# Kernel tuning notes

Hardware: AMD Instinct MI355X
Metric: run time of the kernel (lower is better)

## Reference

```python
import jax, jax.numpy as jnp
import numpy as np

N_NODES = 20000
NEG_SLOPE = 0.2  # PyG GATConv default leaky_relu slope


def segment_softmax(e, dst, num_segments):
    # e: [E, H] edge logits, softmax over edges sharing the same dst node
    m = jax.ops.segment_max(e, dst, num_segments=num_segments)
    ex = jnp.exp(e - m[dst])
    s = jax.ops.segment_sum(ex, dst, num_segments=num_segments)
    return ex / (s[dst] + 1e-16)


def gat_conv(x, src, dst, W, att_src, att_dst, bias, concat):
    # PyG GATConv (add_self_loops handled by caller). W: [Fin, H*C], att_*: [H, C]
    N = x.shape[0]
    H, C = att_src.shape
    h = (x @ W).reshape(N, H, C)
    a_src = jnp.einsum('nhc,hc->nh', h, att_src)  # [N, H]
    a_dst = jnp.einsum('nhc,hc->nh', h, att_dst)
    e = jax.nn.leaky_relu(a_src[src] + a_dst[dst], NEG_SLOPE)  # [E, H]
    alpha = segment_softmax(e, dst, N)
    msg = alpha[:, :, None] * h[src]  # [E, H, C]
    out = jax.ops.segment_sum(msg, dst, num_segments=N)  # [N, H, C]
    out = out.reshape(N, H * C) if concat else out.mean(axis=1)
    return out + bias


def add_self_loops(edge_index, num_nodes):
    loops = jnp.arange(num_nodes, dtype=edge_index.dtype)
    src = jnp.concatenate([edge_index[0], loops])
    dst = jnp.concatenate([edge_index[1], loops])
    return src, dst


def setup_inputs() -> dict:
    key = jax.random.key(0)
    ks = jax.random.split(key, 24)
    Fin, Hd, Hh, C2, Md = 1280, 256, 4, 128, 1024

    def w(k, shape, fan_in):
        return (jax.random.normal(k, shape, jnp.float32) * (1.0 / np.sqrt(fan_in))).astype(jnp.float32)

    return {
        'x': jax.random.normal(ks[0], (N_NODES, Fin), jnp.float32),
        'edge_index': jax.random.randint(ks[1], (2, 200000), 0, N_NODES, jnp.int32),
        'mutation_idx': 12345,
        'mutation_site_diff': jax.random.normal(ks[2], (1, Md), jnp.float32),
        # mutation_diff_processor: 1024 -> 128 -> 128
        'W_mut1': w(ks[3], (Md, 128), Md), 'b_mut1': jnp.zeros((128,), jnp.float32),
        'W_mut2': w(ks[4], (128, 128), 128), 'b_mut2': jnp.zeros((128,), jnp.float32),
        # GATConv1: Fin -> 256, 4 heads, concat
        'gat1_W': w(ks[5], (Fin, Hh * Hd), Fin),
        'gat1_as': w(ks[6], (Hh, Hd), Hd), 'gat1_ad': w(ks[7], (Hh, Hd), Hd),
        'gat1_b': jnp.zeros((Hh * Hd,), jnp.float32),
        # GATConv2: 1024 -> 128, 1 head
        'gat2_W': w(ks[8], (Hh * Hd, C2), Hh * Hd),
        'gat2_as': w(ks[9], (1, C2), C2), 'gat2_ad': w(ks[10], (1, C2), C2),
        'gat2_b': jnp.zeros((C2,), jnp.float32),
        # binding_predictor: 256 -> 128 -> 32 -> 1
        'W_p1': w(ks[11], (C2 + 128, 128), C2 + 128), 'b_p1': jnp.zeros((128,), jnp.float32),
        'W_p2': w(ks[12], (128, 32), 128), 'b_p2': jnp.zeros((32,), jnp.float32),
        'W_p3': w(ks[13], (32, 1), 32), 'b_p3': jnp.zeros((1,), jnp.float32),
    }


def reference(x, edge_index, mutation_idx, mutation_site_diff,
              W_mut1, b_mut1, W_mut2, b_mut2,
              gat1_W, gat1_as, gat1_ad, gat1_b,
              gat2_W, gat2_as, gat2_ad, gat2_b,
              W_p1, b_p1, W_p2, b_p2, W_p3, b_p3):
    src, dst = add_self_loops(edge_index, x.shape[0])
    # mutation diff MLP (dropout = identity at eval)
    pmd = jax.nn.relu(mutation_site_diff @ W_mut1 + b_mut1) @ W_mut2 + b_mut2
    h = jax.nn.relu(gat_conv(x, src, dst, gat1_W, gat1_as, gat1_ad, gat1_b, concat=True))
    h = jax.nn.relu(gat_conv(h, src, dst, gat2_W, gat2_as, gat2_ad, gat2_b, concat=False))
    feat = h[mutation_idx:mutation_idx + 1]  # [1, 128]
    z = jnp.concatenate([feat, pmd], axis=-1)
    z = jax.nn.relu(z @ W_p1 + b_p1)
    z = jax.nn.relu(z @ W_p2 + b_p2)
    return z @ W_p3 + b_p3
```

## Files before the change

### kernel.cpp

```cpp
#include <hip/hip_runtime.h>
#include <hip/hip_bf16.h>

#define NNODES 20000
#define NE_RAW 200000
#define NE_TOT 220000
#define MAX1   128
#define MAX2   512
#define MAXE1  4096
#define MAXE2  256
#define FIN    1280
#define FH     1024
#define HC     256
#define NHEAD  4
#define C2     128
#define CAPE   512
#define GB_HH  544
#define GB_GB  128

__device__ __forceinline__ float lrelu(float x){ return x >= 0.f ? x : 0.2f * x; }

__device__ __forceinline__ float blockSum(float v, float* red4){
  #pragma unroll
  for (int o = 32; o; o >>= 1) v += __shfl_xor(v, o, 64);
  int t = threadIdx.x;
  __syncthreads();
  if ((t & 63) == 0) red4[t >> 6] = v;
  __syncthreads();
  return red4[0] + red4[1] + red4[2] + red4[3];
}

__global__ void k_init(int* cnt, int* slot1, int* slot2){
  int i = blockIdx.x * 256 + threadIdx.x;
  if (i < NNODES){ slot1[i] = -1; slot2[i] = -1; }
  if (i < 8) cnt[i] = 0;
}

__global__ void k_scan1(const int* __restrict__ ei, const int* __restrict__ mip,
                        int* cnt, int* slot1, int* S1, int* E2){
  int e = blockIdx.x * 256 + threadIdx.x;
  if (e >= NE_TOT) return;
  int mi = mip[0];
  int src, dst;
  if (e < NE_RAW){ src = ei[e]; dst = ei[NE_RAW + e]; }
  else { src = e - NE_RAW; dst = src; }
  if (dst != mi) return;
  int p = atomicAdd(&cnt[3], 1);
  if (p < MAXE2) E2[p] = src;
  if (atomicCAS(&slot1[src], -1, -9) == -1){
    int idx = atomicAdd(&cnt[0], 1);
    if (idx < MAX1){ S1[idx] = src; slot1[src] = idx; }
  }
}

__global__ void k_scan2(const int* __restrict__ ei, int* cnt,
                        const int* __restrict__ slot1, int* slot2,
                        int* S2, int* E1s, int* E1d){
  int e = blockIdx.x * 256 + threadIdx.x;
  if (e >= NE_TOT) return;
  int src, dst;
  if (e < NE_RAW){ src = ei[e]; dst = ei[NE_RAW + e]; }
  else { src = e - NE_RAW; dst = src; }
  if (slot1[dst] < 0) return;
  int p = atomicAdd(&cnt[2], 1);
  if (p < MAXE1){ E1s[p] = src; E1d[p] = dst; }
  if (atomicCAS(&slot2[src], -1, -9) == -1){
    int idx = atomicAdd(&cnt[1], 1);
    if (idx < MAX2){ S2[idx] = src; slot2[src] = idx; }
  }
}

__global__ __launch_bounds__(256) void k_hh(
    const float* __restrict__ x, const float* __restrict__ W1,
    const float* __restrict__ msd, const float* __restrict__ Wm1,
    const float* __restrict__ bm1,
    const int* __restrict__ cnt, const int* __restrict__ S2,
    float* __restrict__ hh, float* __restrict__ r1){
  int t = threadIdx.x;
  if (blockIdx.x >= GB_HH){
    __shared__ float red[256];
    int b   = blockIdx.x - GB_HH;
    int col = b * 32 + (t & 31);
    int sl  = t >> 5;
    float p = 0.f;
    for (int k = sl * 128; k < sl * 128 + 128; ++k)
      p += msd[k] * Wm1[k * C2 + col];
    red[t] = p;
    __syncthreads();
    if (t < 32){
      float s = 0.f;
      #pragma unroll
      for (int q = 0; q < 8; ++q) s += red[q * 32 + t];
      float v = s + bm1[col];
      r1[col] = v > 0.f ? v : 0.f;
    }
    return;
  }
  __shared__ float xs[8 * 160];
  int n2 = cnt[1]; if (n2 > MAX2) n2 = MAX2;
  int nRG = (n2 + 7) >> 3;
  int nT  = nRG * 32;
  for (int task = blockIdx.x; task < nT; task += GB_HH){
    int rg  = task >> 5;
    int rem = task & 31;
    int ct  = rem >> 3;
    int kc  = rem & 7;
    int r0  = rg * 8;
    int nr  = n2 - r0; if (nr > 8) nr = 8;
    int k0  = kc * 160;
    __syncthreads();
    for (int idx = t; idx < 8 * 40; idx += 256){
      int r = idx / 40, k4 = idx - r * 40;
      float4 v = make_float4(0.f, 0.f, 0.f, 0.f);
      if (r < nr)
        v = *(const float4*)(x + (long)S2[r0 + r] * FIN + k0 + k4 * 4);
      *(float4*)(xs + r * 160 + k4 * 4) = v;
    }
    __syncthreads();
    int col = ct * 256 + t;
    float acc[8] = {0.f,0.f,0.f,0.f,0.f,0.f,0.f,0.f};
    const float* Wp = W1 + (long)k0 * FH + col;
    #pragma unroll 4
    for (int kk = 0; kk < 160; ++kk){
      float w = Wp[(long)kk * FH];
      #pragma unroll
      for (int r = 0; r < 8; ++r) acc[r] += xs[r * 160 + kk] * w;
    }
    #pragma unroll
    for (int r = 0; r < 8; ++r)
      if (r < nr) atomicAdd(hh + (long)(r0 + r) * FH + col, acc[r]);
  }
}

__global__ void k_ascal(const float* __restrict__ hh,
                        const float* __restrict__ as1, const float* __restrict__ ad1,
                        const int* __restrict__ cnt,
                        float* __restrict__ asrc1, float* __restrict__ adst1){
  int t = threadIdx.x, w = t >> 6, lane = t & 63;
  int n2 = cnt[1]; if (n2 > MAX2) n2 = MAX2;
  for (int i = blockIdx.x; i < n2; i += gridDim.x){
    const float* row = hh + (long)i * FH + w * HC;
    float ss = 0.f, sd = 0.f;
    #pragma unroll
    for (int q = 0; q < 4; ++q){
      float v = row[q * 64 + lane];
      ss += v * as1[w * HC + q * 64 + lane];
      sd += v * ad1[w * HC + q * 64 + lane];
    }
    #pragma unroll
    for (int o = 32; o; o >>= 1){
      ss += __shfl_xor(ss, o, 64);
      sd += __shfl_xor(sd, o, 64);
    }
    if (lane == 0){ asrc1[i * NHEAD + w] = ss; adst1[i * NHEAD + w] = sd; }
  }
}

__global__ void k_agg1(const float* __restrict__ hh,
                       const float* __restrict__ asrc1, const float* __restrict__ adst1,
                       const float* __restrict__ b1,
                       const int* __restrict__ cnt, const int* __restrict__ S1,
                       const int* __restrict__ slot2,
                       const int* __restrict__ E1s, const int* __restrict__ E1d,
                       float* __restrict__ h1){
  __shared__ int   lsrc[CAPE];
  __shared__ float ev[CAPE];
  __shared__ int   scnt;
  int t = threadIdx.x;
  int n1  = cnt[0]; if (n1  > MAX1)  n1  = MAX1;
  int nE1 = cnt[2]; if (nE1 > MAXE1) nE1 = MAXE1;
  int nT = n1 * NHEAD;
  for (int task = blockIdx.x; task < nT; task += gridDim.x){
    int j = task >> 2, hd = task & 3;
    int s = S1[j];
    __syncthreads();
    if (t == 0) scnt = 0;
    __syncthreads();
    for (int e = t; e < nE1; e += 256){
      if (E1d[e] == s){
        int p = atomicAdd(&scnt, 1);
        if (p < CAPE) lsrc[p] = slot2[E1s[e]];
      }
    }
    __syncthreads();
    int ce = scnt; if (ce > CAPE) ce = CAPE;
    if (t < 64){
      float ad = adst1[slot2[s] * NHEAD + hd];
      float m = -3.4e38f;
      for (int e = t; e < ce; e += 64){
        float v = lrelu(asrc1[lsrc[e] * NHEAD + hd] + ad);
        ev[e] = v;
        m = fmaxf(m, v);
      }
      #pragma unroll
      for (int o = 32; o; o >>= 1) m = fmaxf(m, __shfl_xor(m, o, 64));
      float ssum = 0.f;
      for (int e = t; e < ce; e += 64){
        float a = expf(ev[e] - m);
        ev[e] = a;
        ssum += a;
      }
      #pragma unroll
      for (int o = 32; o; o >>= 1) ssum += __shfl_xor(ssum, o, 64);
      float inv = 1.f / (ssum + 1e-16f);
      for (int e = t; e < ce; e += 64) ev[e] *= inv;
    }
    __syncthreads();
    int c = hd * HC + t;
    float acc = 0.f;
    for (int e = 0; e < ce; ++e)
      acc += ev[e] * hh[(long)lsrc[e] * FH + c];
    float v = acc + b1[c];
    h1[(long)j * FH + c] = v > 0.f ? v : 0.f;
    __syncthreads();
  }
}

__global__ __launch_bounds__(256) void k_gb(
    const float* __restrict__ h1, const float* __restrict__ W2,
    const int* __restrict__ cnt, float* __restrict__ gb){
  __shared__ float hs[128];
  int t = threadIdx.x;
  int n1 = cnt[0]; if (n1 > MAX1) n1 = MAX1;
  int nT = n1 * 8;
  for (int task = blockIdx.x; task < nT; task += GB_GB){
    int j  = task >> 3;
    int kc = task & 7;
    int k0 = kc * 128;
    __syncthreads();
    if (t < 128) hs[t] = h1[(long)j * FH + k0 + t];
    __syncthreads();
    int col = t & 127, sub = t >> 7;
    const float* Wp = W2 + (long)(k0 + sub * 64) * C2 + col;
    const float* hp = hs + sub * 64;
    float acc = 0.f;
    #pragma unroll 16
    for (int i = 0; i < 64; ++i)
      acc += hp[i] * Wp[(long)i * C2];
    atomicAdd(gb + j * C2 + col, acc);
  }
}

__global__ void k_final(const int* __restrict__ mip, const int* __restrict__ cnt,
                        const int* __restrict__ slot1, const int* __restrict__ E2,
                        const float* __restrict__ gb,
                        const float* __restrict__ as2, const float* __restrict__ ad2,
                        const float* __restrict__ b2,
                        const float* __restrict__ r1,
                        const float* __restrict__ Wm2, const float* __restrict__ bm2,
                        const float* __restrict__ Wp1, const float* __restrict__ bp1,
                        const float* __restrict__ Wp2, const float* __restrict__ bp2,
                        const float* __restrict__ Wp3, const float* __restrict__ bp3,
                        float* __restrict__ out){
  __shared__ float al[MAXE2];
  __shared__ int   jl[MAXE2];
  __shared__ float red4[4];
  __shared__ float feat[C2], r2s[C2], z1s[C2], z2s[32];
  int t = threadIdx.x;
  int mi  = mip[0];
  int jmi = slot1[mi];
  int ne2 = cnt[3]; if (ne2 > MAXE2) ne2 = MAXE2;
  for (int k = t; k < ne2; k += 256) jl[k] = slot1[E2[k]];
  __syncthreads();
  float vd = (t < C2) ? gb[jmi * C2 + t] * ad2[t] : 0.f;
  float adv = blockSum(vd, red4);
  for (int k = 0; k < ne2; ++k){
    float vs = (t < C2) ? gb[jl[k] * C2 + t] * as2[t] : 0.f;
    float s = blockSum(vs, red4);
    if (t == 0) al[k] = lrelu(s + adv);
    __syncthreads();
  }
  if (t < 64){
    float m = -3.4e38f;
    for (int k = t; k < ne2; k += 64) m = fmaxf(m, al[k]);
    #pragma unroll
    for (int o = 32; o; o >>= 1) m = fmaxf(m, __shfl_xor(m, o, 64));
    float s = 0.f;
    for (int k = t; k < ne2; k += 64){
      float a = expf(al[k] - m);
      al[k] = a;
      s += a;
    }
    #pragma unroll
    for (int o = 32; o; o >>= 1) s += __shfl_xor(s, o, 64);
    float inv = 1.f / (s + 1e-16f);
    for (int k = t; k < ne2; k += 64) al[k] *= inv;
  }
  __syncthreads();
  if (t < C2){
    float acc = 0.f;
    for (int k = 0; k < ne2; ++k) acc += al[k] * gb[jl[k] * C2 + t];
    float v = acc + b2[t];
    feat[t] = v > 0.f ? v : 0.f;
    float pr = 0.f;
    for (int k = 0; k < C2; ++k) pr += r1[k] * Wm2[k * C2 + t];
    r2s[t] = pr + bm2[t];
  }
  __syncthreads();
  if (t < C2){
    float acc = 0.f;
    for (int k = 0; k < C2; ++k) acc += feat[k] * Wp1[k * C2 + t];
    for (int k = 0; k < C2; ++k) acc += r2s[k] * Wp1[(C2 + k) * C2 + t];
    float v = acc + bp1[t];
    z1s[t] = v > 0.f ? v : 0.f;
  }
  __syncthreads();
  if (t < 32){
    float acc = 0.f;
    for (int k = 0; k < C2; ++k) acc += z1s[k] * Wp2[k * 32 + t];
    float v = acc + bp2[t];
    z2s[t] = v > 0.f ? v : 0.f;
  }
  __syncthreads();
  if (t == 0){
    float acc = 0.f;
    for (int k = 0; k < 32; ++k) acc += z2s[k] * Wp3[k];
    out[0] = acc + bp3[0];
  }
}

extern "C" void kernel_launch(void* const* d_in, const int* in_sizes, int n_in,
                              void* d_out, int out_size, void* d_ws, size_t ws_size,
                              hipStream_t stream){
  const float* x   = (const float*)d_in[0];
  const int*   ei  = (const int*)d_in[1];
  const int*   mip = (const int*)d_in[2];
  const float* msd = (const float*)d_in[3];
  const float* Wm1 = (const float*)d_in[4];
  const float* bm1 = (const float*)d_in[5];
  const float* Wm2 = (const float*)d_in[6];
  const float* bm2 = (const float*)d_in[7];
  const float* W1  = (const float*)d_in[8];
  const float* as1 = (const float*)d_in[9];
  const float* ad1 = (const float*)d_in[10];
  const float* b1  = (const float*)d_in[11];
  const float* W2  = (const float*)d_in[12];
  const float* as2 = (const float*)d_in[13];
  const float* ad2 = (const float*)d_in[14];
  const float* b2  = (const float*)d_in[15];
  const float* Wp1 = (const float*)d_in[16];
  const float* bp1 = (const float*)d_in[17];
  const float* Wp2 = (const float*)d_in[18];
  const float* bp2 = (const float*)d_in[19];
  const float* Wp3 = (const float*)d_in[20];
  const float* bp3 = (const float*)d_in[21];
  float* out = (float*)d_out;

  char* p = (char*)d_ws;
  auto alloc = [&](size_t bytes) -> void* {
    void* r = (void*)p;
    p += (bytes + 255) & ~(size_t)255;
    return r;
  };
  int* cnt   = (int*)alloc(8 * 4);
  int* slot1 = (int*)alloc(NNODES * 4);
  int* slot2 = (int*)alloc(NNODES * 4);
  int* S1    = (int*)alloc(MAX1 * 4);
  int* S2    = (int*)alloc(MAX2 * 4);
  int* E1s   = (int*)alloc(MAXE1 * 4);
  int* E1d   = (int*)alloc(MAXE1 * 4);
  int* E2    = (int*)alloc(MAXE2 * 4);
  float* hh    = (float*)alloc((size_t)MAX2 * FH * 4);
  float* gb    = (float*)alloc(MAX1 * C2 * 4);
  float* asrc1 = (float*)alloc(MAX2 * NHEAD * 4);
  float* adst1 = (float*)alloc(MAX2 * NHEAD * 4);
  float* h1    = (float*)alloc((size_t)MAX1 * FH * 4);
  float* r1    = (float*)alloc(C2 * 4);

  hipMemsetAsync(hh, 0, (size_t)MAX2 * FH * 4 + 256 + MAX1 * C2 * 4, stream);
  k_init<<<(NNODES + 255) / 256, 256, 0, stream>>>(cnt, slot1, slot2);
  k_scan1<<<(NE_TOT + 255) / 256, 256, 0, stream>>>(ei, mip, cnt, slot1, S1, E2);
  k_scan2<<<(NE_TOT + 255) / 256, 256, 0, stream>>>(ei, cnt, slot1, slot2, S2, E1s, E1d);
  k_hh<<<GB_HH + 4, 256, 0, stream>>>(x, W1, msd, Wm1, bm1, cnt, S2, hh, r1);
  k_ascal<<<160, 256, 0, stream>>>(hh, as1, ad1, cnt, asrc1, adst1);
  k_agg1<<<64, 256, 0, stream>>>(hh, asrc1, adst1, b1, cnt, S1, slot2, E1s, E1d, h1);
  k_gb<<<GB_GB, 256, 0, stream>>>(h1, W2, cnt, gb);
  k_final<<<1, 256, 0, stream>>>(mip, cnt, slot1, E2, gb, as2, ad2, b2, r1,
                                 Wm2, bm2, Wp1, bp1, Wp2, bp2, Wp3, bp3, out);
}
```

Before: 61.58 us.

## Retile hh GEMM into split-K partials, fuse aggregation with W2 projection

The first-layer GEMM over gathered rows now uses 64-row tiles with 32 accumulators per thread. Each K-chunk writes its partial into a separate buffer instead of issuing atomicAdds. k_ascal reduces the partials into hh while computing the attention scalars, which removes the memset. k_agg1 now handles all four heads per node and applies the W2 projection in shared memory, which eliminates k_gb, the h1 buffer and its atomics. k_final computes the per-edge attention logits wave-parallel instead of one block reduction per edge. The costs are more partial-buffer traffic and higher register pressure in the GEMM.

```diff
diff --git a/kernel.cpp b/kernel.cpp
--- a/kernel.cpp
+++ b/kernel.cpp
@@ -14,20 +14,13 @@
 #define NHEAD  4
 #define C2     128
 #define CAPE   512
-#define GB_HH  544
-#define GB_GB  128
+#define NKC    8
+#define KCH    160
+#define NCT    8
+#define RG     64
+#define HH_GEMM_BLOCKS 192
 
 __device__ __forceinline__ float lrelu(float x){ return x >= 0.f ? x : 0.2f * x; }
-
-__device__ __forceinline__ float blockSum(float v, float* red4){
-  #pragma unroll
-  for (int o = 32; o; o >>= 1) v += __shfl_xor(v, o, 64);
-  int t = threadIdx.x;
-  __syncthreads();
-  if ((t & 63) == 0) red4[t >> 6] = v;
-  __syncthreads();
-  return red4[0] + red4[1] + red4[2] + red4[3];
-}
 
 __global__ void k_init(int* cnt, int* slot1, int* slot2){
   int i = blockIdx.x * 256 + threadIdx.x;
@@ -74,169 +67,164 @@
     const float* __restrict__ msd, const float* __restrict__ Wm1,
     const float* __restrict__ bm1,
     const int* __restrict__ cnt, const int* __restrict__ S2,
-    float* __restrict__ hh, float* __restrict__ r1){
+    float* __restrict__ hpart, float* __restrict__ r1){
   int t = threadIdx.x;
-  if (blockIdx.x >= GB_HH){
+  if (blockIdx.x >= HH_GEMM_BLOCKS){
     __shared__ float red[256];
-    int b   = blockIdx.x - GB_HH;
+    int b   = blockIdx.x - HH_GEMM_BLOCKS;
     int col = b * 32 + (t & 31);
     int sl  = t >> 5;
-    float p = 0.f;
+    float s = 0.f;
     for (int k = sl * 128; k < sl * 128 + 128; ++k)
-      p += msd[k] * Wm1[k * C2 + col];
-    red[t] = p;
+      s += msd[k] * Wm1[k * C2 + col];
+    red[t] = s;
     __syncthreads();
     if (t < 32){
-      float s = 0.f;
+      float v = 0.f;
       #pragma unroll
-      for (int q = 0; q < 8; ++q) s += red[q * 32 + t];
-      float v = s + bm1[col];
+      for (int q = 0; q < 8; ++q) v += red[q * 32 + t];
+      v += bm1[col];
       r1[col] = v > 0.f ? v : 0.f;
     }
     return;
   }
-  __shared__ float xs[8 * 160];
+  __shared__ float xs[RG * KCH];
   int n2 = cnt[1]; if (n2 > MAX2) n2 = MAX2;
-  int nRG = (n2 + 7) >> 3;
-  int nT  = nRG * 32;
-  for (int task = blockIdx.x; task < nT; task += GB_HH){
-    int rg  = task >> 5;
-    int rem = task & 31;
-    int ct  = rem >> 3;
-    int kc  = rem & 7;
-    int r0  = rg * 8;
-    int nr  = n2 - r0; if (nr > 8) nr = 8;
-    int k0  = kc * 160;
-    __syncthreads();
-    for (int idx = t; idx < 8 * 40; idx += 256){
-      int r = idx / 40, k4 = idx - r * 40;
+  int nRG = (n2 + RG - 1) / RG;
+  int nT  = nRG * NKC * NCT;
+  for (int task = blockIdx.x; task < nT; task += HH_GEMM_BLOCKS){
+    int rg = task >> 6, rem = task & 63;
+    int kc = rem >> 3,  ct  = rem & 7;
+    int r0 = rg * RG,   k0  = kc * KCH;
+    __syncthreads();
+    for (int idx = t; idx < RG * (KCH / 4); idx += 256){
+      int r = idx / (KCH / 4), k4 = idx - r * (KCH / 4);
       float4 v = make_float4(0.f, 0.f, 0.f, 0.f);
-      if (r < nr)
+      if (r0 + r < n2)
         v = *(const float4*)(x + (long)S2[r0 + r] * FIN + k0 + k4 * 4);
-      *(float4*)(xs + r * 160 + k4 * 4) = v;
-    }
-    __syncthreads();
-    int col = ct * 256 + t;
-    float acc[8] = {0.f,0.f,0.f,0.f,0.f,0.f,0.f,0.f};
-    const float* Wp = W1 + (long)k0 * FH + col;
+      *(float4*)(xs + r * KCH + k4 * 4) = v;
+    }
+    __syncthreads();
+    int col = t & 127, rh = t >> 7;
+    float acc[32];
+    #pragma unroll
+    for (int r = 0; r < 32; ++r) acc[r] = 0.f;
+    const float* Wp = W1 + (long)k0 * FH + ct * 128 + col;
+    const float* xp = xs + rh * 32 * KCH;
     #pragma unroll 4
-    for (int kk = 0; kk < 160; ++kk){
+    for (int kk = 0; kk < KCH; ++kk){
       float w = Wp[(long)kk * FH];
       #pragma unroll
-      for (int r = 0; r < 8; ++r) acc[r] += xs[r * 160 + kk] * w;
-    }
-    #pragma unroll
-    for (int r = 0; r < 8; ++r)
-      if (r < nr) atomicAdd(hh + (long)(r0 + r) * FH + col, acc[r]);
-  }
-}
-
-__global__ void k_ascal(const float* __restrict__ hh,
+      for (int r = 0; r < 32; ++r) acc[r] += xp[r * KCH + kk] * w;
+    }
+    float* d0 = hpart + ((long)kc * MAX2 + r0 + rh * 32) * FH + ct * 128 + col;
+    #pragma unroll
+    for (int r = 0; r < 32; ++r)
+      if (r0 + rh * 32 + r < n2) d0[(long)r * FH] = acc[r];
+  }
+}
+
+__global__ void k_ascal(const float* __restrict__ hpart,
                         const float* __restrict__ as1, const float* __restrict__ ad1,
                         const int* __restrict__ cnt,
+                        float* __restrict__ hh,
                         float* __restrict__ asrc1, float* __restrict__ adst1){
-  int t = threadIdx.x, w = t >> 6, lane = t & 63;
+  int t = threadIdx.x, head = t >> 6;
   int n2 = cnt[1]; if (n2 > MAX2) n2 = MAX2;
+  float4 a = *(const float4*)(as1 + 4 * t);
+  float4 d = *(const float4*)(ad1 + 4 * t);
   for (int i = blockIdx.x; i < n2; i += gridDim.x){
-    const float* row = hh + (long)i * FH + w * HC;
-    float ss = 0.f, sd = 0.f;
-    #pragma unroll
-    for (int q = 0; q < 4; ++q){
-      float v = row[q * 64 + lane];
-      ss += v * as1[w * HC + q * 64 + lane];
-      sd += v * ad1[w * HC + q * 64 + lane];
-    }
-    #pragma unroll
-    for (int o = 32; o; o >>= 1){
-      ss += __shfl_xor(ss, o, 64);
-      sd += __shfl_xor(sd, o, 64);
-    }
-    if (lane == 0){ asrc1[i * NHEAD + w] = ss; adst1[i * NHEAD + w] = sd; }
+    float4 s = make_float4(0.f, 0.f, 0.f, 0.f);
+    #pragma unroll
+    for (int kc = 0; kc < NKC; ++kc){
+      float4 v = *(const float4*)(hpart + ((long)kc * MAX2 + i) * FH + 4 * t);
+      s.x += v.x; s.y += v.y; s.z += v.z; s.w += v.w;
+    }
+    *(float4*)(hh + (long)i * FH + 4 * t) = s;
+    float ss = s.x * a.x + s.y * a.y + s.z * a.z + s.w * a.w;
+    float sd = s.x * d.x + s.y * d.y + s.z * d.z + s.w * d.w;
+    #pragma unroll
+    for (int o = 32; o; o >>= 1){ ss += __shfl_xor(ss, o, 64); sd += __shfl_xor(sd, o, 64); }
+    if ((t & 63) == 0){ asrc1[i * NHEAD + head] = ss; adst1[i * NHEAD + head] = sd; }
   }
 }
 
 __global__ void k_agg1(const float* __restrict__ hh,
                        const float* __restrict__ asrc1, const float* __restrict__ adst1,
-                       const float* __restrict__ b1,
+                       const float* __restrict__ b1, const float* __restrict__ W2,
                        const int* __restrict__ cnt, const int* __restrict__ S1,
                        const int* __restrict__ slot2,
                        const int* __restrict__ E1s, const int* __restrict__ E1d,
-                       float* __restrict__ h1){
+                       float* __restrict__ gb){
   __shared__ int   lsrc[CAPE];
-  __shared__ float ev[CAPE];
+  __shared__ float ev[NHEAD][CAPE];
+  __shared__ float h1row[FH];
+  __shared__ float comb[C2];
   __shared__ int   scnt;
   int t = threadIdx.x;
   int n1  = cnt[0]; if (n1  > MAX1)  n1  = MAX1;
   int nE1 = cnt[2]; if (nE1 > MAXE1) nE1 = MAXE1;
-  int nT = n1 * NHEAD;
-  for (int task = blockIdx.x; task < nT; task += gridDim.x){
-    int j = task >> 2, hd = task & 3;
+  for (int j = blockIdx.x; j < n1; j += gridDim.x){
     int s = S1[j];
     __syncthreads();
     if (t == 0) scnt = 0;
     __syncthreads();
     for (int e = t; e < nE1; e += 256){
       if (E1d[e] == s){
-        int p = atomicAdd(&scnt, 1);
-        if (p < CAPE) lsrc[p] = slot2[E1s[e]];
+        int q = atomicAdd(&scnt, 1);
+        if (q < CAPE) lsrc[q] = slot2[E1s[e]];
       }
     }
     __syncthreads();
     int ce = scnt; if (ce > CAPE) ce = CAPE;
-    if (t < 64){
-      float ad = adst1[slot2[s] * NHEAD + hd];
+    int w = t >> 6, lane = t & 63;
+    {
+      float ad = adst1[slot2[s] * NHEAD + w];
       float m = -3.4e38f;
-      for (int e = t; e < ce; e += 64){
-        float v = lrelu(asrc1[lsrc[e] * NHEAD + hd] + ad);
-        ev[e] = v;
+      for (int e = lane; e < ce; e += 64){
+        float v = lrelu(asrc1[lsrc[e] * NHEAD + w] + ad);
+        ev[w][e] = v;
         m = fmaxf(m, v);
       }
       #pragma unroll
       for (int o = 32; o; o >>= 1) m = fmaxf(m, __shfl_xor(m, o, 64));
       float ssum = 0.f;
-      for (int e = t; e < ce; e += 64){
-        float a = expf(ev[e] - m);
-        ev[e] = a;
-        ssum += a;
+      for (int e = lane; e < ce; e += 64){
+        float a2 = expf(ev[w][e] - m);
+        ev[w][e] = a2;
+        ssum += a2;
       }
       #pragma unroll
       for (int o = 32; o; o >>= 1) ssum += __shfl_xor(ssum, o, 64);
       float inv = 1.f / (ssum + 1e-16f);
-      for (int e = t; e < ce; e += 64) ev[e] *= inv;
-    }
-    __syncthreads();
-    int c = hd * HC + t;
-    float acc = 0.f;
-    for (int e = 0; e < ce; ++e)
-      acc += ev[e] * hh[(long)lsrc[e] * FH + c];
-    float v = acc + b1[c];
-    h1[(long)j * FH + c] = v > 0.f ? v : 0.f;
-    __syncthreads();
-  }
-}
-
-__global__ __launch_bounds__(256) void k_gb(
-    const float* __restrict__ h1, const float* __restrict__ W2,
-    const int* __restrict__ cnt, float* __restrict__ gb){
-  __shared__ float hs[128];
-  int t = threadIdx.x;
-  int n1 = cnt[0]; if (n1 > MAX1) n1 = MAX1;
-  int nT = n1 * 8;
-  for (int task = blockIdx.x; task < nT; task += GB_GB){
-    int j  = task >> 3;
-    int kc = task & 7;
-    int k0 = kc * 128;
-    __syncthreads();
-    if (t < 128) hs[t] = h1[(long)j * FH + k0 + t];
+      for (int e = lane; e < ce; e += 64) ev[w][e] *= inv;
+    }
+    __syncthreads();
+    float4 accv = make_float4(0.f, 0.f, 0.f, 0.f);
+    int hd = t >> 6;
+    for (int e = 0; e < ce; ++e){
+      float al = ev[hd][e];
+      float4 hv = *(const float4*)(hh + (long)lsrc[e] * FH + 4 * t);
+      accv.x += al * hv.x; accv.y += al * hv.y; accv.z += al * hv.z; accv.w += al * hv.w;
+    }
+    float4 bv = *(const float4*)(b1 + 4 * t);
+    accv.x += bv.x; accv.y += bv.y; accv.z += bv.z; accv.w += bv.w;
+    accv.x = accv.x > 0.f ? accv.x : 0.f;
+    accv.y = accv.y > 0.f ? accv.y : 0.f;
+    accv.z = accv.z > 0.f ? accv.z : 0.f;
+    accv.w = accv.w > 0.f ? accv.w : 0.f;
+    *(float4*)(h1row + 4 * t) = accv;
     __syncthreads();
     int col = t & 127, sub = t >> 7;
-    const float* Wp = W2 + (long)(k0 + sub * 64) * C2 + col;
-    const float* hp = hs + sub * 64;
-    float acc = 0.f;
-    #pragma unroll 16
-    for (int i = 0; i < 64; ++i)
-      acc += hp[i] * Wp[(long)i * C2];
-    atomicAdd(gb + j * C2 + col, acc);
+    float g = 0.f;
+    const float* Wp = W2 + (long)(sub * 512) * C2 + col;
+    const float* hp = h1row + sub * 512;
+    #pragma unroll 8
+    for (int k = 0; k < 512; ++k) g += hp[k] * Wp[(long)k * C2];
+    if (sub == 1) comb[col] = g;
+    __syncthreads();
+    if (sub == 0) gb[j * C2 + col] = g + comb[col];
+    __syncthreads();
   }
 }
 
@@ -253,7 +241,6 @@
                         float* __restrict__ out){
   __shared__ float al[MAXE2];
   __shared__ int   jl[MAXE2];
-  __shared__ float red4[4];
   __shared__ float feat[C2], r2s[C2], z1s[C2], z2s[32];
   int t = threadIdx.x;
   int mi  = mip[0];
@@ -261,14 +248,24 @@
   int ne2 = cnt[3]; if (ne2 > MAXE2) ne2 = MAXE2;
   for (int k = t; k < ne2; k += 256) jl[k] = slot1[E2[k]];
   __syncthreads();
-  float vd = (t < C2) ? gb[jmi * C2 + t] * ad2[t] : 0.f;
-  float adv = blockSum(vd, red4);
-  for (int k = 0; k < ne2; ++k){
-    float vs = (t < C2) ? gb[jl[k] * C2 + t] * as2[t] : 0.f;
-    float s = blockSum(vs, red4);
-    if (t == 0) al[k] = lrelu(s + adv);
-    __syncthreads();
-  }
+  int w = t >> 6, lane = t & 63;
+  float adv;
+  {
+    int c = lane * 2;
+    float v = gb[jmi * C2 + c] * ad2[c] + gb[jmi * C2 + c + 1] * ad2[c + 1];
+    #pragma unroll
+    for (int o = 32; o; o >>= 1) v += __shfl_xor(v, o, 64);
+    adv = v;
+  }
+  for (int k = w; k < ne2; k += 4){
+    int c = lane * 2;
+    int jj = jl[k];
+    float v = gb[jj * C2 + c] * as2[c] + gb[jj * C2 + c + 1] * as2[c + 1];
+    #pragma unroll
+    for (int o = 32; o; o >>= 1) v += __shfl_xor(v, o, 64);
+    if (lane == 0) al[k] = lrelu(v + adv);
+  }
+  __syncthreads();
   if (t < 64){
     float m = -3.4e38f;
     for (int k = t; k < ne2; k += 64) m = fmaxf(m, al[k]);
@@ -276,9 +273,9 @@
     for (int o = 32; o; o >>= 1) m = fmaxf(m, __shfl_xor(m, o, 64));
     float s = 0.f;
     for (int k = t; k < ne2; k += 64){
-      float a = expf(al[k] - m);
-      al[k] = a;
-      s += a;
+      float a2 = expf(al[k] - m);
+      al[k] = a2;
+      s += a2;
     }
     #pragma unroll
     for (int o = 32; o; o >>= 1) s += __shfl_xor(s, o, 64);
@@ -345,10 +342,10 @@
   const float* bp3 = (const float*)d_in[21];
   float* out = (float*)d_out;
 
-  char* p = (char*)d_ws;
+  char* q = (char*)d_ws;
   auto alloc = [&](size_t bytes) -> void* {
-    void* r = (void*)p;
-    p += (bytes + 255) & ~(size_t)255;
+    void* r = (void*)q;
+    q += (bytes + 255) & ~(size_t)255;
     return r;
   };
   int* cnt   = (int*)alloc(8 * 4);
@@ -359,21 +356,19 @@
   int* E1s   = (int*)alloc(MAXE1 * 4);
   int* E1d   = (int*)alloc(MAXE1 * 4);
   int* E2    = (int*)alloc(MAXE2 * 4);
+  float* hpart = (float*)alloc((size_t)NKC * MAX2 * FH * 4);
   float* hh    = (float*)alloc((size_t)MAX2 * FH * 4);
   float* gb    = (float*)alloc(MAX1 * C2 * 4);
   float* asrc1 = (float*)alloc(MAX2 * NHEAD * 4);
   float* adst1 = (float*)alloc(MAX2 * NHEAD * 4);
-  float* h1    = (float*)alloc((size_t)MAX1 * FH * 4);
   float* r1    = (float*)alloc(C2 * 4);
 
-  hipMemsetAsync(hh, 0, (size_t)MAX2 * FH * 4 + 256 + MAX1 * C2 * 4, stream);
-  k_init<<<(NNODES + 255) / 256, 256, 0, stream>>>(cnt, slot1, slot2);
+  k_init <<<(NNODES + 255) / 256, 256, 0, stream>>>(cnt, slot1, slot2);
   k_scan1<<<(NE_TOT + 255) / 256, 256, 0, stream>>>(ei, mip, cnt, slot1, S1, E2);
   k_scan2<<<(NE_TOT + 255) / 256, 256, 0, stream>>>(ei, cnt, slot1, slot2, S2, E1s, E1d);
-  k_hh<<<GB_HH + 4, 256, 0, stream>>>(x, W1, msd, Wm1, bm1, cnt, S2, hh, r1);
-  k_ascal<<<160, 256, 0, stream>>>(hh, as1, ad1, cnt, asrc1, adst1);
-  k_agg1<<<64, 256, 0, stream>>>(hh, asrc1, adst1, b1, cnt, S1, slot2, E1s, E1d, h1);
-  k_gb<<<GB_GB, 256, 0, stream>>>(h1, W2, cnt, gb);
+  k_hh   <<<HH_GEMM_BLOCKS + 4, 256, 0, stream>>>(x, W1, msd, Wm1, bm1, cnt, S2, hpart, r1);
+  k_ascal<<<128, 256, 0, stream>>>(hpart, as1, ad1, cnt, hh, asrc1, adst1);
+  k_agg1 <<<32, 256, 0, stream>>>(hh, asrc1, adst1, b1, W2, cnt, S1, slot2, E1s, E1d, gb);
   k_final<<<1, 256, 0, stream>>>(mip, cnt, slot1, E2, gb, as2, ad2, b2, r1,
                                  Wm2, bm2, Wp1, bp1, Wp2, bp2, Wp3, bp3, out);
 }
```

Result: slower. 101.5 us (+64.8%).
